# Performance work log

Measured on AMD Instinct MI355X. Metric: run time of the kernel, lower is better.

## Reference

```python
import jax, jax.numpy as jnp
import numpy as np

SEQ, D_IN, D_OUT = 8192, 1024, 1024

def setup_inputs() -> dict:
    key = jax.random.key(0)
    kx, kq, kk, kv = jax.random.split(key, 4)
    scale = 1.0 / np.sqrt(D_IN)
    return {
        "x": jax.random.normal(kx, (SEQ, D_IN), dtype=jnp.float32),
        "Wq": jax.random.normal(kq, (D_OUT, D_IN), dtype=jnp.float32) * scale,
        "Wk": jax.random.normal(kk, (D_OUT, D_IN), dtype=jnp.float32) * scale,
        "Wv": jax.random.normal(kv, (D_OUT, D_IN), dtype=jnp.float32) * scale,
    }

def reference(x, Wq, Wk, Wv):
    # nn.Linear: y = x @ W.T (no bias)
    q = x @ Wq.T            # [S, d_out]
    k = x @ Wk.T            # [S, d_out]
    v = x @ Wv.T            # [S, d_out]
    d_k = k.shape[-1]
    scores = (q @ k.T) / jnp.sqrt(jnp.float32(d_k))   # [S, S]
    attn = jax.nn.softmax(scores, axis=-1)
    return attn @ v         # [S, d_out]
```

## Files before the change

kernel.cpp:

```cpp
#include <hip/hip_runtime.h>

typedef unsigned short ushort_t;
typedef __attribute__((ext_vector_type(8))) __bf16 bf16x8;
typedef __attribute__((ext_vector_type(4))) float f32x4;

#define SEQ 8192
#define DIN 1024
#define DOUT 1024

#define OM_BF16 0
#define OM_EXP  2
#define OM_NORM 3

__device__ __forceinline__ ushort_t f2bf(float f) {
  union { float f; unsigned u; } c; c.f = f;
  unsigned u = c.u;
  return (ushort_t)((u + 0x7fffu + ((u >> 16) & 1u)) >> 16);
}

__device__ __forceinline__ void async16(ushort_t* lds, const ushort_t* g) {
  __builtin_amdgcn_global_load_lds(
      (__attribute__((address_space(1))) void*)g,
      (__attribute__((address_space(3))) void*)lds, 16, 0, 0);
}

template <int N>
__device__ __forceinline__ void waitv() {
  asm volatile("s_waitcnt vmcnt(%0)" :: "n"(N) : "memory");
}

__device__ __forceinline__ int fsw(int row) { return (row ^ (row >> 2)) & 3; }

__global__ __launch_bounds__(256) void cvt_all_kernel(
    const float* __restrict__ x, const float* __restrict__ wq,
    const float* __restrict__ wk, const float* __restrict__ wv,
    ushort_t* __restrict__ xb, ushort_t* __restrict__ wqkb,
    ushort_t* __restrict__ wvb) {
  int b = blockIdx.x;
  const float* src;
  ushort_t* dst;
  int idx;
  if (b < 8192) {
    src = x; dst = xb; idx = b * 256 + threadIdx.x;
  } else {
    int r = b - 8192;
    int w = r >> 10;
    idx = (r & 1023) * 256 + threadIdx.x;
    if (w == 0)      { src = wq; dst = wqkb; }
    else if (w == 1) { src = wk; dst = wqkb + DOUT * DIN; }
    else             { src = wv; dst = wvb; }
  }
  float4 f = ((const float4*)src)[idx];
  ushort4 o;
  o.x = f2bf(f.x); o.y = f2bf(f.y); o.z = f2bf(f.z); o.w = f2bf(f.w);
  ((ushort4*)dst)[idx] = o;
}

__global__ __launch_bounds__(256) void rowsum_inv_kernel(const float* __restrict__ rsp,
                                                         float* __restrict__ invrs) {
  int r = blockIdx.x * 256 + threadIdx.x;
  float s = 0.f;
  #pragma unroll
  for (int p2 = 0; p2 < 32; ++p2) s += rsp[p2 * SEQ + r];
  invrs[r] = 1.0f / s;
}

template <int OUTMODE, int BN>
__global__ __launch_bounds__(512, 2) void gemm256(
    const ushort_t* __restrict__ A, const ushort_t* __restrict__ B,
    void* __restrict__ C, int lda, int ldb, int ldc, int K, float scale,
    float* __restrict__ rsp, const float* __restrict__ invrs) {
  constexpr int BKS = 32;
  constexpr int NIN = BN / 64;
  constexpr int NA = 2;
  constexpr int NB = BN * 4 / 512;
  constexpr int LPG = NA + NB;
  constexpr int AST = 256 * BKS;
  constexpr int BST = BN * BKS;
  __shared__ ushort_t As[4 * AST];
  __shared__ ushort_t Bs[4 * BST];

  const int t = threadIdx.x;
  const int lane = t & 63;
  const int wave = t >> 6;
  const int wr = wave >> 2, wc = wave & 3;
  const int quad = lane >> 4, r16 = lane & 15;

  const int gx = gridDim.x;
  const int nwg = gx * gridDim.y;
  const int bid = blockIdx.y * gx + blockIdx.x;
  const int q8 = nwg >> 3;
  const int b2 = (bid & 7) * q8 + (bid >> 3);
  const int mt = b2 / gx;
  const int nt = b2 - mt * gx;
  const int rowBase = mt * 256;
  const int colBase = nt * BN;

  unsigned offA[NA], offB[NB];
  #pragma unroll
  for (int i = 0; i < NA; ++i) {
    int c = t + i * 512, row = c >> 2, sl = c & 3;
    offA[i] = (unsigned)((rowBase + row) * lda + ((sl ^ fsw(row)) << 3));
  }
  #pragma unroll
  for (int i = 0; i < NB; ++i) {
    int c = t + i * 512, row = c >> 2, sl = c & 3;
    offB[i] = (unsigned)((colBase + row) * ldb + ((sl ^ fsw(row)) << 3));
  }

  f32x4 acc[8][NIN] = {};

  const int NS = K / BKS;

  #pragma unroll
  for (int s = 0; s < 3; ++s) {
    #pragma unroll
    for (int i = 0; i < NA; ++i) {
      async16(&As[s * AST + (t + i * 512) * 8], A + offA[i]); offA[i] += BKS;
    }
    #pragma unroll
    for (int i = 0; i < NB; ++i) {
      async16(&Bs[s * BST + (t + i * 512) * 8], B + offB[i]); offB[i] += BKS;
    }
  }

  for (int s = 0; s < NS; ++s) {
    const int rem = NS - 1 - s;
    if (rem >= 2)      waitv<2 * LPG>();
    else if (rem == 1) waitv<LPG>();
    else               waitv<0>();
    __builtin_amdgcn_s_barrier();
    asm volatile("" ::: "memory");
    __builtin_amdgcn_sched_barrier(0);

    const ushort_t* as = &As[(s & 3) * AST];
    const ushort_t* bs = &Bs[(s & 3) * BST];
    bf16x8 af[8], bfr[NIN];
    #pragma unroll
    for (int mi = 0; mi < 8; ++mi) {
      int row = wr * 128 + mi * 16 + r16;
      int sl = quad ^ fsw(row);
      af[mi] = *(const bf16x8*)&as[(row * 4 + sl) * 8];
    }
    #pragma unroll
    for (int ni = 0; ni < NIN; ++ni) {
      int row = wc * (BN / 4) + ni * 16 + r16;
      int sl = quad ^ fsw(row);
      bfr[ni] = *(const bf16x8*)&bs[(row * 4 + sl) * 8];
    }

    if (s + 3 < NS) {
      const int sb = (s + 3) & 3;
      #pragma unroll
      for (int i = 0; i < NA; ++i) {
        async16(&As[sb * AST + (t + i * 512) * 8], A + offA[i]); offA[i] += BKS;
      }
      #pragma unroll
      for (int i = 0; i < NB; ++i) {
        async16(&Bs[sb * BST + (t + i * 512) * 8], B + offB[i]); offB[i] += BKS;
      }
    }

    __builtin_amdgcn_s_setprio(1);
    #pragma unroll
    for (int mi = 0; mi < 8; ++mi)
      #pragma unroll
      for (int ni = 0; ni < NIN; ++ni)
        acc[mi][ni] = __builtin_amdgcn_mfma_f32_16x16x32_bf16(af[mi], bfr[ni],
                                                              acc[mi][ni], 0, 0, 0);
    __builtin_amdgcn_s_setprio(0);
    __builtin_amdgcn_sched_barrier(0);
  }

  float iv[8][4];
  if constexpr (OUTMODE == OM_NORM) {
    #pragma unroll
    for (int mi = 0; mi < 8; ++mi)
      #pragma unroll
      for (int r = 0; r < 4; ++r)
        iv[mi][r] = invrs[rowBase + wr * 128 + mi * 16 + quad * 4 + r];
  }

  float psum[8][4];
  if constexpr (OUTMODE == OM_EXP) {
    #pragma unroll
    for (int mi = 0; mi < 8; ++mi)
      #pragma unroll
      for (int r = 0; r < 4; ++r) psum[mi][r] = 0.f;
  }

  #pragma unroll
  for (int mi = 0; mi < 8; ++mi)
    #pragma unroll
    for (int ni = 0; ni < NIN; ++ni)
      #pragma unroll
      for (int r = 0; r < 4; ++r) {
        int grow = rowBase + wr * 128 + mi * 16 + quad * 4 + r;
        int gcol = colBase + wc * (BN / 4) + ni * 16 + r16;
        float a = acc[mi][ni][r];
        if constexpr (OUTMODE == OM_BF16) {
          ((ushort_t*)C)[(size_t)grow * ldc + gcol] = f2bf(a * scale);
        } else if constexpr (OUTMODE == OM_EXP) {
          float e = exp2f(a * scale);
          psum[mi][r] += e;
          ((ushort_t*)C)[(size_t)grow * ldc + gcol] = f2bf(e);
        } else {
          ((float*)C)[(size_t)grow * ldc + gcol] = a * iv[mi][r];
        }
      }

  if constexpr (OUTMODE == OM_EXP) {
    __syncthreads();
    float* lds_rs = (float*)As;
    #pragma unroll
    for (int mi = 0; mi < 8; ++mi)
      #pragma unroll
      for (int r = 0; r < 4; ++r) {
        float sv = psum[mi][r];
        sv += __shfl_xor(sv, 1, 64);
        sv += __shfl_xor(sv, 2, 64);
        sv += __shfl_xor(sv, 4, 64);
        sv += __shfl_xor(sv, 8, 64);
        if (r16 == 0)
          lds_rs[wc * 256 + wr * 128 + mi * 16 + quad * 4 + r] = sv;
      }
    __syncthreads();
    if (t < 256)
      rsp[(size_t)nt * SEQ + rowBase + t] =
          lds_rs[t] + lds_rs[256 + t] + lds_rs[512 + t] + lds_rs[768 + t];
  }
}

extern "C" void kernel_launch(void* const* d_in, const int* in_sizes, int n_in,
                              void* d_out, int out_size, void* d_ws, size_t ws_size,
                              hipStream_t stream) {
  const float* x  = (const float*)d_in[0];
  const float* Wq = (const float*)d_in[1];
  const float* Wk = (const float*)d_in[2];
  const float* Wv = (const float*)d_in[3];
  float* out = (float*)d_out;

  char* p = (char*)d_ws;
  ushort_t* xb   = (ushort_t*)p; p += (size_t)SEQ * DIN * 2;
  ushort_t* wqkb = (ushort_t*)p; p += (size_t)2 * DOUT * DIN * 2;
  ushort_t* wvb  = (ushort_t*)p; p += (size_t)DOUT * DIN * 2;
  ushort_t* qkb  = (ushort_t*)p; p += (size_t)SEQ * 2 * DOUT * 2;
  ushort_t* vtb  = (ushort_t*)p; p += (size_t)DOUT * SEQ * 2;
  float*    rsp  = (float*)p;    p += (size_t)64 * SEQ * 4;
  float*    irs  = (float*)p;    p += (size_t)SEQ * 4;
  ushort_t* Sb   = (ushort_t*)p; p += (size_t)SEQ * SEQ * 2;

  cvt_all_kernel<<<8192 + 3 * 1024, 256, 0, stream>>>(x, Wq, Wk, Wv, xb, wqkb, wvb);

  dim3 blk(512);
  gemm256<OM_BF16, 256><<<dim3(2048 / 256, SEQ / 256), blk, 0, stream>>>(
      xb, wqkb, qkb, DIN, DIN, 2 * DOUT, DIN, 1.0f, nullptr, nullptr);

  gemm256<OM_BF16, 128><<<dim3(SEQ / 128, DOUT / 256), blk, 0, stream>>>(
      wvb, xb, vtb, DIN, DIN, SEQ, DIN, 1.0f, nullptr, nullptr);

  gemm256<OM_EXP, 256><<<dim3(SEQ / 256, SEQ / 256), blk, 0, stream>>>(
      qkb, qkb + DOUT, Sb, 2 * DOUT, 2 * DOUT, SEQ, DIN,
      0.03125f * 1.44269504f, rsp, nullptr);

  rowsum_inv_kernel<<<SEQ / 256, 256, 0, stream>>>(rsp, irs);

  gemm256<OM_NORM, 128><<<dim3(DOUT / 128, SEQ / 256), blk, 0, stream>>>(
      Sb, vtb, out, SEQ, SEQ, DOUT, SEQ, 1.0f, nullptr, irs);
}
```

Before: 475.1 us.

## Split GEMM main loop into two half-phases and add supertile block swizzle for QK^T

The GEMM inner step is split into two halves. The first half loads four A fragments and the B fragments, issues the A prefetch and runs half the MFMAs. The second half then loads the remaining A fragments, issues the B prefetch and runs the rest, with explicit lgkmcnt waits and an extra barrier between them. The aim is to overlap LDS reads and global-to-LDS prefetch with MFMA work and cut register pressure. The score GEMM also gets a hierarchical block-to-tile mapping meant to improve L2 reuse across XCDs. In exchange, each K step adds a barrier, and the mapping hard-codes a 32x32 tile grid.

```diff
diff --git a/kernel.cpp b/kernel.cpp
--- a/kernel.cpp
+++ b/kernel.cpp
@@ -27,6 +27,11 @@
 template <int N>
 __device__ __forceinline__ void waitv() {
   asm volatile("s_waitcnt vmcnt(%0)" :: "n"(N) : "memory");
+}
+
+__device__ __forceinline__ void waitlgkm0() {
+  asm volatile("s_waitcnt lgkmcnt(0)" ::: "memory");
+  __builtin_amdgcn_sched_barrier(0);
 }
 
 __device__ __forceinline__ int fsw(int row) { return (row ^ (row >> 2)) & 3; }
@@ -65,7 +70,7 @@
   invrs[r] = 1.0f / s;
 }
 
-template <int OUTMODE, int BN>
+template <int OUTMODE, int SUPER, int BN>
 __global__ __launch_bounds__(512, 2) void gemm256(
     const ushort_t* __restrict__ A, const ushort_t* __restrict__ B,
     void* __restrict__ C, int lda, int ldb, int ldc, int K, float scale,
@@ -89,10 +94,17 @@
   const int gx = gridDim.x;
   const int nwg = gx * gridDim.y;
   const int bid = blockIdx.y * gx + blockIdx.x;
-  const int q8 = nwg >> 3;
-  const int b2 = (bid & 7) * q8 + (bid >> 3);
-  const int mt = b2 / gx;
-  const int nt = b2 - mt * gx;
+  int mt, nt;
+  if (SUPER == 1) {
+    int x = bid & 7, l = bid >> 3;
+    mt = ((x >> 2) << 4) + ((l >> 5) << 2) + ((l >> 3) & 3);
+    nt = ((x & 3) << 3) + (l & 7);
+  } else {
+    const int q8 = nwg >> 3;
+    const int b2 = (bid & 7) * q8 + (bid >> 3);
+    mt = b2 / gx;
+    nt = b2 - mt * gx;
+  }
   const int rowBase = mt * 256;
   const int colBase = nt * BN;
 
@@ -130,44 +142,62 @@
     else if (rem == 1) waitv<LPG>();
     else               waitv<0>();
     __builtin_amdgcn_s_barrier();
-    asm volatile("" ::: "memory");
     __builtin_amdgcn_sched_barrier(0);
 
     const ushort_t* as = &As[(s & 3) * AST];
     const ushort_t* bs = &Bs[(s & 3) * BST];
-    bf16x8 af[8], bfr[NIN];
-    #pragma unroll
-    for (int mi = 0; mi < 8; ++mi) {
+    const bool pf = (s + 3 < NS);
+    const int sb = (s + 3) & 3;
+
+    bf16x8 af0[4], bfr[NIN];
+    #pragma unroll
+    for (int mi = 0; mi < 4; ++mi) {
       int row = wr * 128 + mi * 16 + r16;
-      int sl = quad ^ fsw(row);
-      af[mi] = *(const bf16x8*)&as[(row * 4 + sl) * 8];
+      af0[mi] = *(const bf16x8*)&as[(row * 4 + (quad ^ fsw(row))) * 8];
     }
     #pragma unroll
     for (int ni = 0; ni < NIN; ++ni) {
       int row = wc * (BN / 4) + ni * 16 + r16;
-      int sl = quad ^ fsw(row);
-      bfr[ni] = *(const bf16x8*)&bs[(row * 4 + sl) * 8];
-    }
-
-    if (s + 3 < NS) {
-      const int sb = (s + 3) & 3;
+      bfr[ni] = *(const bf16x8*)&bs[(row * 4 + (quad ^ fsw(row))) * 8];
+    }
+    if (pf) {
       #pragma unroll
       for (int i = 0; i < NA; ++i) {
         async16(&As[sb * AST + (t + i * 512) * 8], A + offA[i]); offA[i] += BKS;
       }
+    }
+    waitlgkm0();
+    __builtin_amdgcn_s_setprio(1);
+    #pragma unroll
+    for (int mi = 0; mi < 4; ++mi)
+      #pragma unroll
+      for (int ni = 0; ni < NIN; ++ni)
+        acc[mi][ni] = __builtin_amdgcn_mfma_f32_16x16x32_bf16(af0[mi], bfr[ni],
+                                                              acc[mi][ni], 0, 0, 0);
+    __builtin_amdgcn_s_setprio(0);
+    __builtin_amdgcn_sched_barrier(0);
+
+    bf16x8 af1[4];
+    #pragma unroll
+    for (int mi = 0; mi < 4; ++mi) {
+      int row = wr * 128 + 64 + mi * 16 + r16;
+      af1[mi] = *(const bf16x8*)&as[(row * 4 + (quad ^ fsw(row))) * 8];
+    }
+    if (pf) {
       #pragma unroll
       for (int i = 0; i < NB; ++i) {
         async16(&Bs[sb * BST + (t + i * 512) * 8], B + offB[i]); offB[i] += BKS;
       }
     }
-
+    __builtin_amdgcn_s_barrier();
+    waitlgkm0();
     __builtin_amdgcn_s_setprio(1);
     #pragma unroll
-    for (int mi = 0; mi < 8; ++mi)
+    for (int mi = 0; mi < 4; ++mi)
       #pragma unroll
       for (int ni = 0; ni < NIN; ++ni)
-        acc[mi][ni] = __builtin_amdgcn_mfma_f32_16x16x32_bf16(af[mi], bfr[ni],
-                                                              acc[mi][ni], 0, 0, 0);
+        acc[4 + mi][ni] = __builtin_amdgcn_mfma_f32_16x16x32_bf16(af1[mi], bfr[ni],
+                                                                  acc[4 + mi][ni], 0, 0, 0);
     __builtin_amdgcn_s_setprio(0);
     __builtin_amdgcn_sched_barrier(0);
   }
@@ -253,18 +283,18 @@
   cvt_all_kernel<<<8192 + 3 * 1024, 256, 0, stream>>>(x, Wq, Wk, Wv, xb, wqkb, wvb);
 
   dim3 blk(512);
-  gemm256<OM_BF16, 256><<<dim3(2048 / 256, SEQ / 256), blk, 0, stream>>>(
+  gemm256<OM_BF16, 0, 256><<<dim3(2048 / 256, SEQ / 256), blk, 0, stream>>>(
       xb, wqkb, qkb, DIN, DIN, 2 * DOUT, DIN, 1.0f, nullptr, nullptr);
 
-  gemm256<OM_BF16, 128><<<dim3(SEQ / 128, DOUT / 256), blk, 0, stream>>>(
+  gemm256<OM_BF16, 0, 128><<<dim3(SEQ / 128, DOUT / 256), blk, 0, stream>>>(
       wvb, xb, vtb, DIN, DIN, SEQ, DIN, 1.0f, nullptr, nullptr);
 
-  gemm256<OM_EXP, 256><<<dim3(SEQ / 256, SEQ / 256), blk, 0, stream>>>(
+  gemm256<OM_EXP, 1, 256><<<dim3(SEQ / 256, SEQ / 256), blk, 0, stream>>>(
       qkb, qkb + DOUT, Sb, 2 * DOUT, 2 * DOUT, SEQ, DIN,
       0.03125f * 1.44269504f, rsp, nullptr);
 
   rowsum_inv_kernel<<<SEQ / 256, 256, 0, stream>>>(rsp, irs);
 
-  gemm256<OM_NORM, 128><<<dim3(DOUT / 128, SEQ / 256), blk, 0, stream>>>(
+  gemm256<OM_NORM, 0, 128><<<dim3(DOUT / 128, SEQ / 256), blk, 0, stream>>>(
       Sb, vtb, out, SEQ, SEQ, DOUT, SEQ, 1.0f, nullptr, irs);
 }
```

After: 489.8 us. 1.03x slower.

## Rewrite GEMMs to 4-wave 32x32x16 MFMA tiles with BK=64 double buffering

Applied to the files above, without the earlier changes.

Replaces the 8-wave, 16x16x32 MFMA GEMM (BK=32, 4-stage async ring) with a 4-wave kernel that uses 32x32x16 MFMAs, a 64-wide K tile with double buffering, an 8-slot XOR swizzle, and per-wave 128x128 output tiles. It also adds a supertile block-order mapping for the QK^T GEMM and restructures the exp/rowsum epilogue. The goal is more register-level reuse per LDS read and fewer barriers per FLOP. In exchange each wave holds a much larger accumulator, so occupancy drops to one 256-thread block per CU, and the shallower pipeline gives less latency hiding.

```diff
diff --git a/kernel.cpp b/kernel.cpp
--- a/kernel.cpp
+++ b/kernel.cpp
@@ -2,7 +2,7 @@
 
 typedef unsigned short ushort_t;
 typedef __attribute__((ext_vector_type(8))) __bf16 bf16x8;
-typedef __attribute__((ext_vector_type(4))) float f32x4;
+typedef __attribute__((ext_vector_type(16))) float f32x16;
 
 #define SEQ 8192
 #define DIN 1024
@@ -28,8 +28,6 @@
 __device__ __forceinline__ void waitv() {
   asm volatile("s_waitcnt vmcnt(%0)" :: "n"(N) : "memory");
 }
-
-__device__ __forceinline__ int fsw(int row) { return (row ^ (row >> 2)) & 3; }
 
 __global__ __launch_bounds__(256) void cvt_all_kernel(
     const float* __restrict__ x, const float* __restrict__ wq,
@@ -65,169 +63,166 @@
   invrs[r] = 1.0f / s;
 }
 
-template <int OUTMODE, int BN>
-__global__ __launch_bounds__(512, 2) void gemm256(
+template <int OUTMODE, int SUPER, int BM, int BN>
+__global__ __launch_bounds__(256, 1) void gemm4w(
     const ushort_t* __restrict__ A, const ushort_t* __restrict__ B,
     void* __restrict__ C, int lda, int ldb, int ldc, int K, float scale,
     float* __restrict__ rsp, const float* __restrict__ invrs) {
-  constexpr int BKS = 32;
-  constexpr int NIN = BN / 64;
-  constexpr int NA = 2;
-  constexpr int NB = BN * 4 / 512;
+  constexpr int WM = BM / 2, WN = BN / 2;
+  constexpr int MI = WM / 32, NI = WN / 32;
+  constexpr int AST = BM * 64;
+  constexpr int BST = BN * 64;
+  constexpr int NA = BM / 32;
+  constexpr int NB = BN / 32;
   constexpr int LPG = NA + NB;
-  constexpr int AST = 256 * BKS;
-  constexpr int BST = BN * BKS;
-  __shared__ ushort_t As[4 * AST];
-  __shared__ ushort_t Bs[4 * BST];
+  __shared__ ushort_t As[2 * AST];
+  __shared__ ushort_t Bs[2 * BST];
 
   const int t = threadIdx.x;
   const int lane = t & 63;
   const int wave = t >> 6;
-  const int wr = wave >> 2, wc = wave & 3;
-  const int quad = lane >> 4, r16 = lane & 15;
+  const int wrM = wave >> 1, wcN = wave & 1;
+  const int hi = lane >> 5, l5 = lane & 31;
 
   const int gx = gridDim.x;
   const int nwg = gx * gridDim.y;
   const int bid = blockIdx.y * gx + blockIdx.x;
-  const int q8 = nwg >> 3;
-  const int b2 = (bid & 7) * q8 + (bid >> 3);
-  const int mt = b2 / gx;
-  const int nt = b2 - mt * gx;
-  const int rowBase = mt * 256;
+  int mt, nt;
+  if (SUPER == 1) {
+    int x = bid & 7, l = bid >> 3;
+    mt = ((x >> 2) << 4) + ((l >> 5) << 2) + ((l >> 3) & 3);
+    nt = ((x & 3) << 3) + (l & 7);
+  } else {
+    const int q8 = nwg >> 3;
+    const int b2 = (bid & 7) * q8 + (bid >> 3);
+    mt = b2 / gx;
+    nt = b2 - mt * gx;
+  }
+  const int rowBase = mt * BM;
   const int colBase = nt * BN;
 
   unsigned offA[NA], offB[NB];
   #pragma unroll
   for (int i = 0; i < NA; ++i) {
-    int c = t + i * 512, row = c >> 2, sl = c & 3;
-    offA[i] = (unsigned)((rowBase + row) * lda + ((sl ^ fsw(row)) << 3));
+    int c = t + i * 256, row = c >> 3, sl = c & 7;
+    offA[i] = (unsigned)((rowBase + row) * lda + ((sl ^ (row & 7)) << 3));
   }
   #pragma unroll
   for (int i = 0; i < NB; ++i) {
-    int c = t + i * 512, row = c >> 2, sl = c & 3;
-    offB[i] = (unsigned)((colBase + row) * ldb + ((sl ^ fsw(row)) << 3));
-  }
-
-  f32x4 acc[8][NIN] = {};
-
-  const int NS = K / BKS;
-
-  #pragma unroll
-  for (int s = 0; s < 3; ++s) {
-    #pragma unroll
-    for (int i = 0; i < NA; ++i) {
-      async16(&As[s * AST + (t + i * 512) * 8], A + offA[i]); offA[i] += BKS;
+    int c = t + i * 256, row = c >> 3, sl = c & 7;
+    offB[i] = (unsigned)((colBase + row) * ldb + ((sl ^ (row & 7)) << 3));
+  }
+
+  f32x16 acc[MI][NI] = {};
+
+  const int NT = K / 64;
+
+  #pragma unroll
+  for (int i = 0; i < NA; ++i) {
+    async16(&As[(t + i * 256) * 8], A + offA[i]); offA[i] += 64;
+  }
+  #pragma unroll
+  for (int i = 0; i < NB; ++i) {
+    async16(&Bs[(t + i * 256) * 8], B + offB[i]); offB[i] += 64;
+  }
+
+  for (int kt = 0; kt < NT; ++kt) {
+    const int cur = kt & 1;
+    if (kt + 1 < NT) {
+      const int nx = cur ^ 1;
+      #pragma unroll
+      for (int i = 0; i < NA; ++i) {
+        async16(&As[nx * AST + (t + i * 256) * 8], A + offA[i]); offA[i] += 64;
+      }
+      #pragma unroll
+      for (int i = 0; i < NB; ++i) {
+        async16(&Bs[nx * BST + (t + i * 256) * 8], B + offB[i]); offB[i] += 64;
+      }
+      waitv<LPG>();
+    } else {
+      waitv<0>();
     }
-    #pragma unroll
-    for (int i = 0; i < NB; ++i) {
-      async16(&Bs[s * BST + (t + i * 512) * 8], B + offB[i]); offB[i] += BKS;
-    }
-  }
-
-  for (int s = 0; s < NS; ++s) {
-    const int rem = NS - 1 - s;
-    if (rem >= 2)      waitv<2 * LPG>();
-    else if (rem == 1) waitv<LPG>();
-    else               waitv<0>();
     __builtin_amdgcn_s_barrier();
     asm volatile("" ::: "memory");
-    __builtin_amdgcn_sched_barrier(0);
-
-    const ushort_t* as = &As[(s & 3) * AST];
-    const ushort_t* bs = &Bs[(s & 3) * BST];
-    bf16x8 af[8], bfr[NIN];
+
+    const ushort_t* as = As + cur * AST;
+    const ushort_t* bs = Bs + cur * BST;
     #pragma unroll
-    for (int mi = 0; mi < 8; ++mi) {
-      int row = wr * 128 + mi * 16 + r16;
-      int sl = quad ^ fsw(row);
-      af[mi] = *(const bf16x8*)&as[(row * 4 + sl) * 8];
+    for (int ks = 0; ks < 4; ++ks) {
+      bf16x8 a_[MI], b_[NI];
+      #pragma unroll
+      for (int mi = 0; mi < MI; ++mi) {
+        int row = wrM * WM + mi * 32 + l5;
+        int sl = (ks * 2 + hi) ^ (row & 7);
+        a_[mi] = *(const bf16x8*)&as[(row * 8 + sl) * 8];
+      }
+      #pragma unroll
+      for (int ni = 0; ni < NI; ++ni) {
+        int row = wcN * WN + ni * 32 + l5;
+        int sl = (ks * 2 + hi) ^ (row & 7);
+        b_[ni] = *(const bf16x8*)&bs[(row * 8 + sl) * 8];
+      }
+      __builtin_amdgcn_s_setprio(1);
+      #pragma unroll
+      for (int mi = 0; mi < MI; ++mi)
+        #pragma unroll
+        for (int ni = 0; ni < NI; ++ni)
+          acc[mi][ni] = __builtin_amdgcn_mfma_f32_32x32x16_bf16(
+              a_[mi], b_[ni], acc[mi][ni], 0, 0, 0);
+      __builtin_amdgcn_s_setprio(0);
     }
-    #pragma unroll
-    for (int ni = 0; ni < NIN; ++ni) {
-      int row = wc * (BN / 4) + ni * 16 + r16;
-      int sl = quad ^ fsw(row);
-      bfr[ni] = *(const bf16x8*)&bs[(row * 4 + sl) * 8];
-    }
-
-    if (s + 3 < NS) {
-      const int sb = (s + 3) & 3;
-      #pragma unroll
-      for (int i = 0; i < NA; ++i) {
-        async16(&As[sb * AST + (t + i * 512) * 8], A + offA[i]); offA[i] += BKS;
-      }
-      #pragma unroll
-      for (int i = 0; i < NB; ++i) {
-        async16(&Bs[sb * BST + (t + i * 512) * 8], B + offB[i]); offB[i] += BKS;
-      }
-    }
-
-    __builtin_amdgcn_s_setprio(1);
-    #pragma unroll
-    for (int mi = 0; mi < 8; ++mi)
-      #pragma unroll
-      for (int ni = 0; ni < NIN; ++ni)
-        acc[mi][ni] = __builtin_amdgcn_mfma_f32_16x16x32_bf16(af[mi], bfr[ni],
-                                                              acc[mi][ni], 0, 0, 0);
-    __builtin_amdgcn_s_setprio(0);
-    __builtin_amdgcn_sched_barrier(0);
-  }
-
-  float iv[8][4];
+    __builtin_amdgcn_s_barrier();
+    asm volatile("" ::: "memory");
+  }
+
+  float iv_[MI][16];
   if constexpr (OUTMODE == OM_NORM) {
     #pragma unroll
-    for (int mi = 0; mi < 8; ++mi)
-      #pragma unroll
-      for (int r = 0; r < 4; ++r)
-        iv[mi][r] = invrs[rowBase + wr * 128 + mi * 16 + quad * 4 + r];
-  }
-
-  float psum[8][4];
-  if constexpr (OUTMODE == OM_EXP) {
+    for (int mi = 0; mi < MI; ++mi)
+      #pragma unroll
+      for (int g = 0; g < 16; ++g) {
+        int rr = (g & 3) + 8 * (g >> 2) + 4 * hi;
+        iv_[mi][g] = invrs[rowBase + wrM * WM + mi * 32 + rr];
+      }
+  }
+
+  float* lds_rs = (float*)As;
+
+  #pragma unroll
+  for (int mi = 0; mi < MI; ++mi)
     #pragma unroll
-    for (int mi = 0; mi < 8; ++mi)
-      #pragma unroll
-      for (int r = 0; r < 4; ++r) psum[mi][r] = 0.f;
-  }
-
-  #pragma unroll
-  for (int mi = 0; mi < 8; ++mi)
-    #pragma unroll
-    for (int ni = 0; ni < NIN; ++ni)
-      #pragma unroll
-      for (int r = 0; r < 4; ++r) {
-        int grow = rowBase + wr * 128 + mi * 16 + quad * 4 + r;
-        int gcol = colBase + wc * (BN / 4) + ni * 16 + r16;
-        float a = acc[mi][ni][r];
+    for (int g = 0; g < 16; ++g) {
+      int rr = (g & 3) + 8 * (g >> 2) + 4 * hi;
+      int grow = rowBase + wrM * WM + mi * 32 + rr;
+      float s = 0.f;
+      #pragma unroll
+      for (int ni = 0; ni < NI; ++ni) {
+        int gcol = colBase + wcN * WN + ni * 32 + l5;
+        float a = acc[mi][ni][g];
         if constexpr (OUTMODE == OM_BF16) {
           ((ushort_t*)C)[(size_t)grow * ldc + gcol] = f2bf(a * scale);
         } else if constexpr (OUTMODE == OM_EXP) {
           float e = exp2f(a * scale);
-          psum[mi][r] += e;
+          s += e;
           ((ushort_t*)C)[(size_t)grow * ldc + gcol] = f2bf(e);
         } else {
-          ((float*)C)[(size_t)grow * ldc + gcol] = a * iv[mi][r];
+          ((float*)C)[(size_t)grow * ldc + gcol] = a * iv_[mi][g];
         }
       }
+      if constexpr (OUTMODE == OM_EXP) {
+        s += __shfl_xor(s, 1, 64);
+        s += __shfl_xor(s, 2, 64);
+        s += __shfl_xor(s, 4, 64);
+        s += __shfl_xor(s, 8, 64);
+        s += __shfl_xor(s, 16, 64);
+        if (l5 == 0)
+          lds_rs[wcN * 256 + wrM * 128 + mi * 32 + rr] = s;
+      }
+    }
 
   if constexpr (OUTMODE == OM_EXP) {
     __syncthreads();
-    float* lds_rs = (float*)As;
-    #pragma unroll
-    for (int mi = 0; mi < 8; ++mi)
-      #pragma unroll
-      for (int r = 0; r < 4; ++r) {
-        float sv = psum[mi][r];
-        sv += __shfl_xor(sv, 1, 64);
-        sv += __shfl_xor(sv, 2, 64);
-        sv += __shfl_xor(sv, 4, 64);
-        sv += __shfl_xor(sv, 8, 64);
-        if (r16 == 0)
-          lds_rs[wc * 256 + wr * 128 + mi * 16 + quad * 4 + r] = sv;
-      }
-    __syncthreads();
-    if (t < 256)
-      rsp[(size_t)nt * SEQ + rowBase + t] =
-          lds_rs[t] + lds_rs[256 + t] + lds_rs[512 + t] + lds_rs[768 + t];
+    rsp[(size_t)nt * SEQ + rowBase + t] = lds_rs[t] + lds_rs[256 + t];
   }
 }
 
@@ -252,19 +247,19 @@
 
   cvt_all_kernel<<<8192 + 3 * 1024, 256, 0, stream>>>(x, Wq, Wk, Wv, xb, wqkb, wvb);
 
-  dim3 blk(512);
-  gemm256<OM_BF16, 256><<<dim3(2048 / 256, SEQ / 256), blk, 0, stream>>>(
+  dim3 blk(256);
+  gemm4w<OM_BF16, 0, 256, 256><<<dim3(2048 / 256, SEQ / 256), blk, 0, stream>>>(
       xb, wqkb, qkb, DIN, DIN, 2 * DOUT, DIN, 1.0f, nullptr, nullptr);
 
-  gemm256<OM_BF16, 128><<<dim3(SEQ / 128, DOUT / 256), blk, 0, stream>>>(
+  gemm4w<OM_BF16, 0, 128, 256><<<dim3(SEQ / 256, DOUT / 128), blk, 0, stream>>>(
       wvb, xb, vtb, DIN, DIN, SEQ, DIN, 1.0f, nullptr, nullptr);
 
-  gemm256<OM_EXP, 256><<<dim3(SEQ / 256, SEQ / 256), blk, 0, stream>>>(
+  gemm4w<OM_EXP, 1, 256, 256><<<dim3(SEQ / 256, SEQ / 256), blk, 0, stream>>>(
       qkb, qkb + DOUT, Sb, 2 * DOUT, 2 * DOUT, SEQ, DIN,
       0.03125f * 1.44269504f, rsp, nullptr);
 
   rowsum_inv_kernel<<<SEQ / 256, 256, 0, stream>>>(rsp, irs);
 
-  gemm256<OM_NORM, 128><<<dim3(DOUT / 128, SEQ / 256), blk, 0, stream>>>(
+  gemm4w<OM_NORM, 0, 256, 128><<<dim3(DOUT / 128, SEQ / 256), blk, 0, stream>>>(
       Sb, vtb, out, SEQ, SEQ, DOUT, SEQ, 1.0f, nullptr, irs);
 }
```

Result: slower. 583.4 us (+22.8%).

## Rewrite GEMM as 8-phase ping-pong pipeline with BK=64 half-tile staging

Applied to the files above, without the earlier changes.

Replaces the 4-stage BK=32 GEMM loop with a double-buffered BK=64 scheme. Each K-block is split into four phases that interleave half-tile LDS reads, async global-to-LDS loads and MFMA bursts, with barriers between phases. The LDS swizzle moves to 8 slots per row, tile shapes are templated (the V-projection GEMM now uses 128x256 tiles), and the QK^T GEMM gets a supertile block remap for L2 locality. The aim is to hide load latency behind MFMA work and reduce LDS bank conflicts, at the cost of more barriers per iteration and more complex scheduling.

```diff
diff --git a/kernel.cpp b/kernel.cpp
--- a/kernel.cpp
+++ b/kernel.cpp
@@ -28,8 +28,6 @@
 __device__ __forceinline__ void waitv() {
   asm volatile("s_waitcnt vmcnt(%0)" :: "n"(N) : "memory");
 }
-
-__device__ __forceinline__ int fsw(int row) { return (row ^ (row >> 2)) & 3; }
 
 __global__ __launch_bounds__(256) void cvt_all_kernel(
     const float* __restrict__ x, const float* __restrict__ wq,
@@ -65,20 +63,19 @@
   invrs[r] = 1.0f / s;
 }
 
-template <int OUTMODE, int BN>
-__global__ __launch_bounds__(512, 2) void gemm256(
+template <int OUTMODE, int SUPER, int BM, int BN>
+__global__ __launch_bounds__(512, 2) void gemm8p(
     const ushort_t* __restrict__ A, const ushort_t* __restrict__ B,
     void* __restrict__ C, int lda, int ldb, int ldc, int K, float scale,
     float* __restrict__ rsp, const float* __restrict__ invrs) {
-  constexpr int BKS = 32;
-  constexpr int NIN = BN / 64;
-  constexpr int NA = 2;
-  constexpr int NB = BN * 4 / 512;
-  constexpr int LPG = NA + NB;
-  constexpr int AST = 256 * BKS;
-  constexpr int BST = BN * BKS;
-  __shared__ ushort_t As[4 * AST];
-  __shared__ ushort_t Bs[4 * BST];
+  constexpr int WM = BM / 2, WN = BN / 4;
+  constexpr int MI = BM / 32, NIfr = BN / 64;
+  constexpr int MH = MI / 2;
+  constexpr int AST = BM * 64, BST = BN * 64;
+  constexpr int AHALF = AST / 2, BHALF = BST / 2;
+  constexpr int LA = BM / 128, LB = BN / 128;
+  __shared__ ushort_t As[2 * AST];
+  __shared__ ushort_t Bs[2 * BST];
 
   const int t = threadIdx.x;
   const int lane = t & 63;
@@ -89,114 +86,166 @@
   const int gx = gridDim.x;
   const int nwg = gx * gridDim.y;
   const int bid = blockIdx.y * gx + blockIdx.x;
-  const int q8 = nwg >> 3;
-  const int b2 = (bid & 7) * q8 + (bid >> 3);
-  const int mt = b2 / gx;
-  const int nt = b2 - mt * gx;
-  const int rowBase = mt * 256;
+  int mt, nt;
+  if (SUPER == 1) {
+    int x = bid & 7, l = bid >> 3;
+    mt = ((x >> 2) << 4) + ((l >> 5) << 2) + ((l >> 3) & 3);
+    nt = ((x & 3) << 3) + (l & 7);
+  } else {
+    const int q8 = nwg >> 3;
+    const int b2 = (bid & 7) * q8 + (bid >> 3);
+    mt = b2 / gx;
+    nt = b2 - mt * gx;
+  }
+  const int rowBase = mt * BM;
   const int colBase = nt * BN;
 
-  unsigned offA[NA], offB[NB];
+  unsigned offA[2][LA], offB[2][LB];
   #pragma unroll
-  for (int i = 0; i < NA; ++i) {
-    int c = t + i * 512, row = c >> 2, sl = c & 3;
-    offA[i] = (unsigned)((rowBase + row) * lda + ((sl ^ fsw(row)) << 3));
-  }
-  #pragma unroll
-  for (int i = 0; i < NB; ++i) {
-    int c = t + i * 512, row = c >> 2, sl = c & 3;
-    offB[i] = (unsigned)((colBase + row) * ldb + ((sl ^ fsw(row)) << 3));
-  }
-
-  f32x4 acc[8][NIN] = {};
-
-  const int NS = K / BKS;
-
-  #pragma unroll
-  for (int s = 0; s < 3; ++s) {
-    #pragma unroll
-    for (int i = 0; i < NA; ++i) {
-      async16(&As[s * AST + (t + i * 512) * 8], A + offA[i]); offA[i] += BKS;
-    }
-    #pragma unroll
-    for (int i = 0; i < NB; ++i) {
-      async16(&Bs[s * BST + (t + i * 512) * 8], B + offB[i]); offB[i] += BKS;
-    }
-  }
-
-  for (int s = 0; s < NS; ++s) {
-    const int rem = NS - 1 - s;
-    if (rem >= 2)      waitv<2 * LPG>();
-    else if (rem == 1) waitv<LPG>();
-    else               waitv<0>();
+  for (int h = 0; h < 2; ++h) {
+    #pragma unroll
+    for (int i = 0; i < LA; ++i) {
+      int c = t + i * 512, row = c >> 3, sl = c & 7;
+      offA[h][i] = (unsigned)((rowBase + h * (BM / 2) + row) * lda +
+                              ((sl ^ (row & 7)) << 3));
+    }
+    #pragma unroll
+    for (int i = 0; i < LB; ++i) {
+      int c = t + i * 512, row = c >> 3, sl = c & 7;
+      offB[h][i] = (unsigned)((colBase + h * (BN / 2) + row) * ldb +
+                              ((sl ^ (row & 7)) << 3));
+    }
+  }
+
+  auto stageA = [&](int buf, int h) {
+    #pragma unroll
+    for (int i = 0; i < LA; ++i) {
+      async16(&As[buf * AST + h * AHALF + (t + i * 512) * 8], A + offA[h][i]);
+      offA[h][i] += 64;
+    }
+  };
+  auto stageB = [&](int buf, int h) {
+    #pragma unroll
+    for (int i = 0; i < LB; ++i) {
+      async16(&Bs[buf * BST + h * BHALF + (t + i * 512) * 8], B + offB[h][i]);
+      offB[h][i] += 64;
+    }
+  };
+
+  f32x4 acc[MI][NIfr] = {};
+  bf16x8 af[MH], b0[NIfr], b1[NIfr];
+
+  auto readA = [&](const ushort_t* as, int mh, int ks) {
+    #pragma unroll
+    for (int mi = 0; mi < MH; ++mi) {
+      int row = wr * WM + (mh * MH + mi) * 16 + r16;
+      int sl = (ks * 4 + quad) ^ (row & 7);
+      af[mi] = *(const bf16x8*)&as[(row * 8 + sl) * 8];
+    }
+  };
+  auto readB = [&](const ushort_t* bs, int ks, bf16x8* bfr) {
+    #pragma unroll
+    for (int ni = 0; ni < NIfr; ++ni) {
+      int row = wc * WN + ni * 16 + r16;
+      int sl = (ks * 4 + quad) ^ (row & 7);
+      bfr[ni] = *(const bf16x8*)&bs[(row * 8 + sl) * 8];
+    }
+  };
+  auto presync = [&]() {
+    __builtin_amdgcn_sched_barrier(0);
     __builtin_amdgcn_s_barrier();
-    asm volatile("" ::: "memory");
+    asm volatile("s_waitcnt lgkmcnt(0)" ::: "memory");
     __builtin_amdgcn_sched_barrier(0);
-
-    const ushort_t* as = &As[(s & 3) * AST];
-    const ushort_t* bs = &Bs[(s & 3) * BST];
-    bf16x8 af[8], bfr[NIN];
-    #pragma unroll
-    for (int mi = 0; mi < 8; ++mi) {
-      int row = wr * 128 + mi * 16 + r16;
-      int sl = quad ^ fsw(row);
-      af[mi] = *(const bf16x8*)&as[(row * 4 + sl) * 8];
-    }
-    #pragma unroll
-    for (int ni = 0; ni < NIN; ++ni) {
-      int row = wc * (BN / 4) + ni * 16 + r16;
-      int sl = quad ^ fsw(row);
-      bfr[ni] = *(const bf16x8*)&bs[(row * 4 + sl) * 8];
-    }
-
-    if (s + 3 < NS) {
-      const int sb = (s + 3) & 3;
-      #pragma unroll
-      for (int i = 0; i < NA; ++i) {
-        async16(&As[sb * AST + (t + i * 512) * 8], A + offA[i]); offA[i] += BKS;
-      }
-      #pragma unroll
-      for (int i = 0; i < NB; ++i) {
-        async16(&Bs[sb * BST + (t + i * 512) * 8], B + offB[i]); offB[i] += BKS;
-      }
-    }
-
+  };
+  auto mfmaC = [&](int mh, const bf16x8* bfr) {
     __builtin_amdgcn_s_setprio(1);
     #pragma unroll
-    for (int mi = 0; mi < 8; ++mi)
-      #pragma unroll
-      for (int ni = 0; ni < NIN; ++ni)
-        acc[mi][ni] = __builtin_amdgcn_mfma_f32_16x16x32_bf16(af[mi], bfr[ni],
-                                                              acc[mi][ni], 0, 0, 0);
+    for (int mi = 0; mi < MH; ++mi)
+      #pragma unroll
+      for (int ni = 0; ni < NIfr; ++ni)
+        acc[mh * MH + mi][ni] = __builtin_amdgcn_mfma_f32_16x16x32_bf16(
+            af[mi], bfr[ni], acc[mh * MH + mi][ni], 0, 0, 0);
     __builtin_amdgcn_s_setprio(0);
     __builtin_amdgcn_sched_barrier(0);
-  }
-
-  float iv[8][4];
+  };
+
+  stageB(0, 0); stageB(0, 1); stageA(0, 0); stageA(0, 1);
+  stageB(1, 0); stageB(1, 1);
+  waitv<2 * LB>();
+  __builtin_amdgcn_s_barrier();
+
+  const int NITER = K / 128;
+  for (int it = 0; it < NITER; ++it) {
+    const bool more = (it + 1 < NITER);
+    {
+      const ushort_t* as = As;
+      const ushort_t* bs = Bs;
+      readA(as, 0, 0); readB(bs, 0, b0);
+      stageA(1, 0);
+      presync(); mfmaC(0, b0);
+      __builtin_amdgcn_s_barrier();
+      readB(bs, 1, b1); readA(as, 1, 0);
+      stageA(1, 1);
+      presync(); mfmaC(1, b0);
+      __builtin_amdgcn_s_barrier();
+      readA(as, 0, 1);
+      if (more) stageB(0, 0);
+      presync(); mfmaC(0, b1);
+      __builtin_amdgcn_s_barrier();
+      readA(as, 1, 1);
+      if (more) stageB(0, 1);
+      presync(); mfmaC(1, b1);
+      if (more) waitv<2 * LB>(); else waitv<0>();
+      __builtin_amdgcn_s_barrier();
+    }
+    {
+      const ushort_t* as = As + AST;
+      const ushort_t* bs = Bs + BST;
+      readA(as, 0, 0); readB(bs, 0, b0);
+      if (more) stageA(0, 0);
+      presync(); mfmaC(0, b0);
+      __builtin_amdgcn_s_barrier();
+      readB(bs, 1, b1); readA(as, 1, 0);
+      if (more) stageA(0, 1);
+      presync(); mfmaC(1, b0);
+      __builtin_amdgcn_s_barrier();
+      readA(as, 0, 1);
+      if (more) stageB(1, 0);
+      presync(); mfmaC(0, b1);
+      __builtin_amdgcn_s_barrier();
+      readA(as, 1, 1);
+      if (more) stageB(1, 1);
+      presync(); mfmaC(1, b1);
+      if (more) waitv<2 * LB>();
+      __builtin_amdgcn_s_barrier();
+    }
+  }
+
+  float iv[MI][4];
   if constexpr (OUTMODE == OM_NORM) {
     #pragma unroll
-    for (int mi = 0; mi < 8; ++mi)
+    for (int mi = 0; mi < MI; ++mi)
       #pragma unroll
       for (int r = 0; r < 4; ++r)
-        iv[mi][r] = invrs[rowBase + wr * 128 + mi * 16 + quad * 4 + r];
-  }
-
-  float psum[8][4];
+        iv[mi][r] = invrs[rowBase + wr * WM + mi * 16 + quad * 4 + r];
+  }
+
+  float psum[MI][4];
   if constexpr (OUTMODE == OM_EXP) {
     #pragma unroll
-    for (int mi = 0; mi < 8; ++mi)
+    for (int mi = 0; mi < MI; ++mi)
       #pragma unroll
       for (int r = 0; r < 4; ++r) psum[mi][r] = 0.f;
   }
 
   #pragma unroll
-  for (int mi = 0; mi < 8; ++mi)
-    #pragma unroll
-    for (int ni = 0; ni < NIN; ++ni)
+  for (int mi = 0; mi < MI; ++mi)
+    #pragma unroll
+    for (int ni = 0; ni < NIfr; ++ni)
       #pragma unroll
       for (int r = 0; r < 4; ++r) {
-        int grow = rowBase + wr * 128 + mi * 16 + quad * 4 + r;
-        int gcol = colBase + wc * (BN / 4) + ni * 16 + r16;
+        int grow = rowBase + wr * WM + mi * 16 + quad * 4 + r;
+        int gcol = colBase + wc * WN + ni * 16 + r16;
         float a = acc[mi][ni][r];
         if constexpr (OUTMODE == OM_BF16) {
           ((ushort_t*)C)[(size_t)grow * ldc + gcol] = f2bf(a * scale);
@@ -213,7 +262,7 @@
     __syncthreads();
     float* lds_rs = (float*)As;
     #pragma unroll
-    for (int mi = 0; mi < 8; ++mi)
+    for (int mi = 0; mi < MI; ++mi)
       #pragma unroll
       for (int r = 0; r < 4; ++r) {
         float sv = psum[mi][r];
@@ -222,7 +271,7 @@
         sv += __shfl_xor(sv, 4, 64);
         sv += __shfl_xor(sv, 8, 64);
         if (r16 == 0)
-          lds_rs[wc * 256 + wr * 128 + mi * 16 + quad * 4 + r] = sv;
+          lds_rs[wc * 256 + wr * WM + mi * 16 + quad * 4 + r] = sv;
       }
     __syncthreads();
     if (t < 256)
@@ -253,18 +302,18 @@
   cvt_all_kernel<<<8192 + 3 * 1024, 256, 0, stream>>>(x, Wq, Wk, Wv, xb, wqkb, wvb);
 
   dim3 blk(512);
-  gemm256<OM_BF16, 256><<<dim3(2048 / 256, SEQ / 256), blk, 0, stream>>>(
+  gemm8p<OM_BF16, 0, 256, 256><<<dim3(2048 / 256, SEQ / 256), blk, 0, stream>>>(
       xb, wqkb, qkb, DIN, DIN, 2 * DOUT, DIN, 1.0f, nullptr, nullptr);
 
-  gemm256<OM_BF16, 128><<<dim3(SEQ / 128, DOUT / 256), blk, 0, stream>>>(
+  gemm8p<OM_BF16, 0, 128, 256><<<dim3(SEQ / 256, DOUT / 128), blk, 0, stream>>>(
       wvb, xb, vtb, DIN, DIN, SEQ, DIN, 1.0f, nullptr, nullptr);
 
-  gemm256<OM_EXP, 256><<<dim3(SEQ / 256, SEQ / 256), blk, 0, stream>>>(
+  gemm8p<OM_EXP, 1, 256, 256><<<dim3(SEQ / 256, SEQ / 256), blk, 0, stream>>>(
       qkb, qkb + DOUT, Sb, 2 * DOUT, 2 * DOUT, SEQ, DIN,
       0.03125f * 1.44269504f, rsp, nullptr);
 
   rowsum_inv_kernel<<<SEQ / 256, 256, 0, stream>>>(rsp, irs);
 
-  gemm256<OM_NORM, 128><<<dim3(DOUT / 128, SEQ / 256), blk, 0, stream>>>(
+  gemm8p<OM_NORM, 0, 256, 128><<<dim3(DOUT / 128, SEQ / 256), blk, 0, stream>>>(
       Sb, vtb, out, SEQ, SEQ, DOUT, SEQ, 1.0f, nullptr, irs);
 }
```

New measurement: 474.8 us. No clear change (-0.1%).
